# Kernel tuning notes

Measured on AMD Instinct MI355X. Metric: run time of the kernel, lower is better.

Reference implementation:

```python
import jax, jax.numpy as jnp
import numpy as np

N = 1024   # num nodes (assets)
F = 128    # node feature dim (node_dim)
M = 256    # memory_dim (scorer hidden)
E = 8      # edge_dim
BN_EPS = 1e-5


def setup_inputs() -> dict:
    key = jax.random.key(0)
    ks = jax.random.split(key, 6)
    x = jax.random.normal(ks[0], (N, F), dtype=jnp.float32)
    ctx = jax.random.uniform(ks[1], (4,), dtype=jnp.float32)  # [crisis_prob, ttc/30, urgency, confidence]
    W1 = jax.random.normal(ks[2], (M, 2 * F + 4), dtype=jnp.float32) * 0.05
    b1 = jnp.zeros((M,), jnp.float32)
    gamma = jnp.ones((M,), jnp.float32)
    beta = jnp.zeros((M,), jnp.float32)
    run_mean = jnp.zeros((M,), jnp.float32)
    run_var = jnp.ones((M,), jnp.float32)
    W2 = jax.random.normal(ks[3], (E, M), dtype=jnp.float32) * 0.05
    b2 = jnp.zeros((E,), jnp.float32)
    W3 = jax.random.normal(ks[4], (1, E), dtype=jnp.float32) * 0.05
    b3 = jnp.zeros((1,), jnp.float32)
    return {"x": x, "ctx": ctx, "W1": W1, "b1": b1, "gamma": gamma, "beta": beta,
            "run_mean": run_mean, "run_var": run_var, "W2": W2, "b2": b2, "W3": W3, "b3": b3}


def reference(x, ctx, W1, b1, gamma, beta, run_mean, run_var, W2, b2, W3, b3):
    # All unordered pairs i<j (static shapes); original loops over stressed pairs only,
    # we score all pairs and expose the stressed/threshold filter as a boolean mask.
    ii, jj = jnp.triu_indices(N, k=1)  # each [P], P = N*(N-1)/2

    # First linear decomposed: W1 @ [x_i; x_j; ctx] = A x_i + B x_j + (C ctx + b1)
    pa = x @ W1[:, :F].T          # [N, M]
    pb = x @ W1[:, F:2 * F].T     # [N, M]
    cterm = ctx @ W1[:, 2 * F:].T + b1  # [M]

    h = jax.nn.relu(pa[ii] + pb[jj] + cterm)                           # [P, M]
    h = gamma * (h - run_mean) * jax.lax.rsqrt(run_var + BN_EPS) + beta  # eval-mode BatchNorm1d
    h = jax.nn.relu(h @ W2.T + b2)                                     # [P, E]
    scores = jax.nn.sigmoid(h @ W3.T + b3)[:, 0]                       # [P]

    # Stressed-node selection: std over feature dim > mean std (torch unbiased std)
    stress = x.std(axis=1, ddof=1)
    stressed = stress > stress.mean()
    edge_mask = (scores > 0.5) & stressed[ii] & stressed[jj]           # [P] bool
    return scores, edge_mask
```

## Files before the change

kernel.cpp:

```cpp
#include <hip/hip_runtime.h>
#include <math.h>

#define N_NODES 1024
#define F_DIM   128
#define M_DIM   256
#define E_DIM   8
#define P_PAIRS 523776

__global__ __launch_bounds__(256) void kA(const float* __restrict__ x,
                                          const float* __restrict__ ctx,
                                          const float* __restrict__ W1,
                                          const float* __restrict__ b1,
                                          const float* __restrict__ gamma,
                                          const float* __restrict__ beta,
                                          const float* __restrict__ rmean,
                                          const float* __restrict__ rvar,
                                          const float* __restrict__ W2,
                                          const float* __restrict__ b2,
                                          float* __restrict__ pa,
                                          float* __restrict__ pb,
                                          float* __restrict__ stress,
                                          float* __restrict__ cterm,
                                          float* __restrict__ w2ft,
                                          float* __restrict__ b2f) {
  const int t = threadIdx.x;

  if (blockIdx.x == 256) {
    __shared__ float bnbs[256];
    const float c0 = ctx[0], c1 = ctx[1], c2 = ctx[2], c3 = ctx[3];
    const float* row = W1 + (size_t)t * 260 + 256;
    cterm[t] = b1[t] + c0 * row[0] + c1 * row[1] + c2 * row[2] + c3 * row[3];
    const float s   = gamma[t] / sqrtf(rvar[t] + 1e-5f);
    bnbs[t] = beta[t] - s * rmean[t];
    #pragma unroll
    for (int e = 0; e < 8; ++e) w2ft[t * 8 + e] = W2[e * 256 + t] * s;
    __syncthreads();
    const int wv = t >> 6, lane = t & 63;
    #pragma unroll
    for (int r = 0; r < 2; ++r) {
      const int e = wv * 2 + r;
      float acc = 0.f;
      #pragma unroll
      for (int k = 0; k < 4; ++k) acc += W2[e * 256 + lane + 64 * k] * bnbs[lane + 64 * k];
      #pragma unroll
      for (int m = 32; m > 0; m >>= 1) acc += __shfl_xor(acc, m, 64);
      if (lane == 0) b2f[e] = acc + b2[e];
    }
    return;
  }

  __shared__ float xv[4][128];
  const int n0 = blockIdx.x * 4;
  if (t < 128) {
    ((float4*)&xv[0][0])[t] = ((const float4*)(x + (size_t)n0 * F_DIM))[t];
  }
  __syncthreads();

  {
    const int wv = t >> 6, lane = t & 63;
    const float a = xv[wv][lane], b = xv[wv][lane + 64];
    float sum = a + b;
    #pragma unroll
    for (int m = 32; m > 0; m >>= 1) sum += __shfl_xor(sum, m, 64);
    const float mean = sum * (1.0f / 128.0f);
    const float d0 = a - mean, d1 = b - mean;
    float ss = d0 * d0 + d1 * d1;
    #pragma unroll
    for (int m = 32; m > 0; m >>= 1) ss += __shfl_xor(ss, m, 64);
    if (lane == 0) stress[n0 + wv] = sqrtf(ss * (1.0f / 127.0f));
  }

  const int m = t;
  const float4* wrow = (const float4*)(W1 + (size_t)m * 260);
  float accA[4] = {0.f, 0.f, 0.f, 0.f};
  float accB[4] = {0.f, 0.f, 0.f, 0.f};
  #pragma unroll 8
  for (int k4 = 0; k4 < 32; ++k4) {
    const float4 wa = wrow[k4];
    const float4 wb = wrow[32 + k4];
    #pragma unroll
    for (int nn = 0; nn < 4; ++nn) {
      const float4 xf = ((const float4*)&xv[nn][0])[k4];
      accA[nn] = fmaf(xf.w, wa.w, fmaf(xf.z, wa.z, fmaf(xf.y, wa.y, fmaf(xf.x, wa.x, accA[nn]))));
      accB[nn] = fmaf(xf.w, wb.w, fmaf(xf.z, wb.z, fmaf(xf.y, wb.y, fmaf(xf.x, wb.x, accB[nn]))));
    }
  }
  #pragma unroll
  for (int nn = 0; nn < 4; ++nn) {
    pa[(size_t)(n0 + nn) * M_DIM + m] = accA[nn];
    pb[(size_t)(n0 + nn) * M_DIM + m] = accB[nn];
  }
}

__global__ __launch_bounds__(256, 5) void kC(const float* __restrict__ pa,
                                             const float* __restrict__ pb,
                                             const float* __restrict__ cterm,
                                             const float* __restrict__ w2ft,
                                             const float* __restrict__ b2f,
                                             const float* __restrict__ W3,
                                             const float* __restrict__ b3,
                                             const float* __restrict__ stress,
                                             float* __restrict__ out) {
  const int ti = blockIdx.x, tj = blockIdx.y;
  if (tj < ti) return;
  __shared__ float4 a4[32 * 32];
  __shared__ float4 b4[32 * 32];
  const int t  = threadIdx.x;
  const int i0 = ti * 32, j0 = tj * 32;

  float ssum = 0.f;
  {
    const int lane = t & 63;
    #pragma unroll
    for (int k = 0; k < 16; ++k) ssum += stress[lane + 64 * k];
    #pragma unroll
    for (int m = 32; m > 0; m >>= 1) ssum += __shfl_xor(ssum, m, 64);
  }
  const float smean = ssum * (1.0f / 1024.0f);

  const int jx = t & 15;
  const int iy = t >> 4;
  float acc[4][8];
  #pragma unroll
  for (int p = 0; p < 4; ++p)
    #pragma unroll
    for (int e = 0; e < 8; ++e) acc[p][e] = 0.f;

  const float4* pa4 = (const float4*)pa;
  const float4* pb4 = (const float4*)pb;
  const float4* ct4 = (const float4*)cterm;
  const float4* w4g = (const float4*)w2ft;

  for (int cb = 0; cb < 2; ++cb) {
    if (cb) __syncthreads();
    #pragma unroll
    for (int p = 0; p < 4; ++p) {
      const int d  = p * 256 + t;
      const int r  = d >> 5;
      const int dc = d & 31;
      const int c  = (dc - r) & 31;
      const float4 cv = ct4[cb * 32 + c];
      float4 av = pa4[(size_t)(i0 + r) * 64 + cb * 32 + c];
      av.x += cv.x; av.y += cv.y; av.z += cv.z; av.w += cv.w;
      a4[d] = av;
      b4[d] = pb4[(size_t)(j0 + r) * 64 + cb * 32 + c];
    }
    __syncthreads();

    #pragma unroll 2
    for (int m4 = 0; m4 < 32; ++m4) {
      const float4 a0 = a4[iy * 32        + ((m4 + iy) & 31)];
      const float4 a1 = a4[(iy + 16) * 32 + ((m4 + iy + 16) & 31)];
      const float4 b0 = b4[jx * 32        + ((m4 + jx) & 31)];
      const float4 b1 = b4[(jx + 16) * 32 + ((m4 + jx + 16) & 31)];
      float4 w[8];
      #pragma unroll
      for (int q = 0; q < 8; ++q) w[q] = w4g[(cb * 32 + m4) * 8 + q];

      const float* a0f = (const float*)&a0;
      const float* a1f = (const float*)&a1;
      const float* b0f = (const float*)&b0;
      const float* b1f = (const float*)&b1;
      #pragma unroll
      for (int mm = 0; mm < 4; ++mm) {
        const float r00 = fmaxf(a0f[mm] + b0f[mm], 0.f);
        const float r01 = fmaxf(a0f[mm] + b1f[mm], 0.f);
        const float r10 = fmaxf(a1f[mm] + b0f[mm], 0.f);
        const float r11 = fmaxf(a1f[mm] + b1f[mm], 0.f);
        const float* wl = (const float*)&w[mm * 2];
        const float* wh = (const float*)&w[mm * 2 + 1];
        #pragma unroll
        for (int e = 0; e < 4; ++e) {
          acc[0][e]     = fmaf(wl[e], r00, acc[0][e]);
          acc[1][e]     = fmaf(wl[e], r01, acc[1][e]);
          acc[2][e]     = fmaf(wl[e], r10, acc[2][e]);
          acc[3][e]     = fmaf(wl[e], r11, acc[3][e]);
          acc[0][e + 4] = fmaf(wh[e], r00, acc[0][e + 4]);
          acc[1][e + 4] = fmaf(wh[e], r01, acc[1][e + 4]);
          acc[2][e + 4] = fmaf(wh[e], r10, acc[2][e + 4]);
          acc[3][e + 4] = fmaf(wh[e], r11, acc[3][e + 4]);
        }
      }
    }
  }

  float w3v[8], b2v[8];
  #pragma unroll
  for (int e = 0; e < 8; ++e) { w3v[e] = W3[e]; b2v[e] = b2f[e]; }
  const float b3v = b3[0];
  #pragma unroll
  for (int ia = 0; ia < 2; ++ia) {
    #pragma unroll
    for (int jb = 0; jb < 2; ++jb) {
      const int i = i0 + iy + ia * 16;
      const int j = j0 + jx + jb * 16;
      if (i < j) {
        const int p = ia * 2 + jb;
        float logit = b3v;
        #pragma unroll
        for (int e = 0; e < 8; ++e) {
          const float h2 = fmaxf(acc[p][e] + b2v[e], 0.f);
          logit = fmaf(w3v[e], h2, logit);
        }
        const float score = 1.0f / (1.0f + expf(-logit));
        const int idx = i * 1023 - (i * (i - 1)) / 2 + (j - i - 1);
        out[idx] = score;
        const bool mk = (score > 0.5f) && (stress[i] > smean) && (stress[j] > smean);
        out[P_PAIRS + idx] = mk ? 1.0f : 0.0f;
      }
    }
  }
}

extern "C" void kernel_launch(void* const* d_in, const int* in_sizes, int n_in,
                              void* d_out, int out_size, void* d_ws, size_t ws_size,
                              hipStream_t stream) {
  const float* x     = (const float*)d_in[0];
  const float* ctx   = (const float*)d_in[1];
  const float* W1    = (const float*)d_in[2];
  const float* b1    = (const float*)d_in[3];
  const float* gamma = (const float*)d_in[4];
  const float* beta  = (const float*)d_in[5];
  const float* rmean = (const float*)d_in[6];
  const float* rvar  = (const float*)d_in[7];
  const float* W2    = (const float*)d_in[8];
  const float* b2    = (const float*)d_in[9];
  const float* W3    = (const float*)d_in[10];
  const float* b3    = (const float*)d_in[11];
  float* out = (float*)d_out;

  float* ws     = (float*)d_ws;
  float* pa     = ws;
  float* pb     = pa + 262144;
  float* cterm  = pb + 262144;
  float* w2ft   = cterm + 256;
  float* b2f    = w2ft + 2048;
  float* stress = b2f + 8;

  hipLaunchKernelGGL(kA, dim3(257), dim3(256), 0, stream, x, ctx, W1, b1, gamma, beta,
                     rmean, rvar, W2, b2, pa, pb, stress, cterm, w2ft, b2f);
  hipLaunchKernelGGL(kC, dim3(32, 32), dim3(256), 0, stream, pa, pb, cterm, w2ft, b2f,
                     W3, b3, stress, out);
}
```

Baseline: 145.7 us.

## Compact triangular tile grid, fold ctx term into pa, prefetch second chunk

The pair kernel now launches only the 528 upper-triangular 32x32 tiles and recovers (ti,tj) from the linear block index with a sqrt. This replaces the 1024-block grid in which almost half the blocks exited immediately. The context/bias term is now added into pa inside the projection kernel, so the separate cterm buffer and its per-load adds are gone. The second feature chunk is loaded into registers while the first chunk computes, hiding global load latency. The occupancy hint drops from 5 to 4 blocks to make room for the extra prefetch registers, and the inner loop unroll rises to 4.

```diff
diff --git a/kernel.cpp b/kernel.cpp
--- a/kernel.cpp
+++ b/kernel.cpp
@@ -6,6 +6,7 @@
 #define M_DIM   256
 #define E_DIM   8
 #define P_PAIRS 523776
+#define NTILES  528
 
 __global__ __launch_bounds__(256) void kA(const float* __restrict__ x,
                                           const float* __restrict__ ctx,
@@ -20,16 +21,12 @@
                                           float* __restrict__ pa,
                                           float* __restrict__ pb,
                                           float* __restrict__ stress,
-                                          float* __restrict__ cterm,
                                           float* __restrict__ w2ft,
                                           float* __restrict__ b2f) {
   const int t = threadIdx.x;
 
   if (blockIdx.x == 256) {
     __shared__ float bnbs[256];
-    const float c0 = ctx[0], c1 = ctx[1], c2 = ctx[2], c3 = ctx[3];
-    const float* row = W1 + (size_t)t * 260 + 256;
-    cterm[t] = b1[t] + c0 * row[0] + c1 * row[1] + c2 * row[2] + c3 * row[3];
     const float s   = gamma[t] / sqrtf(rvar[t] + 1e-5f);
     bnbs[t] = beta[t] - s * rmean[t];
     #pragma unroll
@@ -85,27 +82,33 @@
       accB[nn] = fmaf(xf.w, wb.w, fmaf(xf.z, wb.z, fmaf(xf.y, wb.y, fmaf(xf.x, wb.x, accB[nn]))));
     }
   }
+  const float c0 = ctx[0], c1 = ctx[1], c2 = ctx[2], c3 = ctx[3];
+  const float* rowt = W1 + (size_t)m * 260 + 256;
+  const float ctv = b1[m] + c0 * rowt[0] + c1 * rowt[1] + c2 * rowt[2] + c3 * rowt[3];
   #pragma unroll
   for (int nn = 0; nn < 4; ++nn) {
-    pa[(size_t)(n0 + nn) * M_DIM + m] = accA[nn];
+    pa[(size_t)(n0 + nn) * M_DIM + m] = accA[nn] + ctv;
     pb[(size_t)(n0 + nn) * M_DIM + m] = accB[nn];
   }
 }
 
-__global__ __launch_bounds__(256, 5) void kC(const float* __restrict__ pa,
+__global__ __launch_bounds__(256, 4) void kC(const float* __restrict__ pa,
                                              const float* __restrict__ pb,
-                                             const float* __restrict__ cterm,
                                              const float* __restrict__ w2ft,
                                              const float* __restrict__ b2f,
                                              const float* __restrict__ W3,
                                              const float* __restrict__ b3,
                                              const float* __restrict__ stress,
                                              float* __restrict__ out) {
-  const int ti = blockIdx.x, tj = blockIdx.y;
-  if (tj < ti) return;
   __shared__ float4 a4[32 * 32];
   __shared__ float4 b4[32 * 32];
-  const int t  = threadIdx.x;
+  const int t = threadIdx.x;
+
+  const int p = blockIdx.x;
+  int tj = (int)((sqrtf(8.0f * (float)p + 1.0f) - 1.0f) * 0.5f);
+  while ((tj + 1) * (tj + 2) / 2 <= p) ++tj;
+  while (tj * (tj + 1) / 2 > p) --tj;
+  const int ti = p - tj * (tj + 1) / 2;
   const int i0 = ti * 32, j0 = tj * 32;
 
   float ssum = 0.f;
@@ -122,32 +125,39 @@
   const int iy = t >> 4;
   float acc[4][8];
   #pragma unroll
-  for (int p = 0; p < 4; ++p)
-    #pragma unroll
-    for (int e = 0; e < 8; ++e) acc[p][e] = 0.f;
+  for (int q = 0; q < 4; ++q)
+    #pragma unroll
+    for (int e = 0; e < 8; ++e) acc[q][e] = 0.f;
 
   const float4* pa4 = (const float4*)pa;
   const float4* pb4 = (const float4*)pb;
-  const float4* ct4 = (const float4*)cterm;
   const float4* w4g = (const float4*)w2ft;
 
-  for (int cb = 0; cb < 2; ++cb) {
-    if (cb) __syncthreads();
-    #pragma unroll
-    for (int p = 0; p < 4; ++p) {
-      const int d  = p * 256 + t;
-      const int r  = d >> 5;
-      const int dc = d & 31;
-      const int c  = (dc - r) & 31;
-      const float4 cv = ct4[cb * 32 + c];
-      float4 av = pa4[(size_t)(i0 + r) * 64 + cb * 32 + c];
-      av.x += cv.x; av.y += cv.y; av.z += cv.z; av.w += cv.w;
-      a4[d] = av;
-      b4[d] = pb4[(size_t)(j0 + r) * 64 + cb * 32 + c];
-    }
-    __syncthreads();
-
-    #pragma unroll 2
+  float4 ra[4], rb[4];
+
+  #pragma unroll
+  for (int q = 0; q < 4; ++q) {
+    const int d = q * 256 + t, r = d >> 5, dc = d & 31, c = (dc - r) & 31;
+    ra[q] = pa4[(size_t)(i0 + r) * 64 + c];
+    rb[q] = pb4[(size_t)(j0 + r) * 64 + c];
+  }
+  #pragma unroll
+  for (int q = 0; q < 4; ++q) {
+    const int d = q * 256 + t;
+    a4[d] = ra[q];
+    b4[d] = rb[q];
+  }
+  __syncthreads();
+
+  #pragma unroll
+  for (int q = 0; q < 4; ++q) {
+    const int d = q * 256 + t, r = d >> 5, dc = d & 31, c = (dc - r) & 31;
+    ra[q] = pa4[(size_t)(i0 + r) * 64 + 32 + c];
+    rb[q] = pb4[(size_t)(j0 + r) * 64 + 32 + c];
+  }
+
+  auto computeChunk = [&](int cw) {
+    #pragma unroll 4
     for (int m4 = 0; m4 < 32; ++m4) {
       const float4 a0 = a4[iy * 32        + ((m4 + iy) & 31)];
       const float4 a1 = a4[(iy + 16) * 32 + ((m4 + iy + 16) & 31)];
@@ -155,7 +165,7 @@
       const float4 b1 = b4[(jx + 16) * 32 + ((m4 + jx + 16) & 31)];
       float4 w[8];
       #pragma unroll
-      for (int q = 0; q < 8; ++q) w[q] = w4g[(cb * 32 + m4) * 8 + q];
+      for (int q = 0; q < 8; ++q) w[q] = w4g[(cw + m4) * 8 + q];
 
       const float* a0f = (const float*)&a0;
       const float* a1f = (const float*)&a1;
@@ -182,7 +192,18 @@
         }
       }
     }
-  }
+  };
+
+  computeChunk(0);
+  __syncthreads();
+  #pragma unroll
+  for (int q = 0; q < 4; ++q) {
+    const int d = q * 256 + t;
+    a4[d] = ra[q];
+    b4[d] = rb[q];
+  }
+  __syncthreads();
+  computeChunk(32);
 
   float w3v[8], b2v[8];
   #pragma unroll
@@ -195,11 +216,11 @@
       const int i = i0 + iy + ia * 16;
       const int j = j0 + jx + jb * 16;
       if (i < j) {
-        const int p = ia * 2 + jb;
+        const int q = ia * 2 + jb;
         float logit = b3v;
         #pragma unroll
         for (int e = 0; e < 8; ++e) {
-          const float h2 = fmaxf(acc[p][e] + b2v[e], 0.f);
+          const float h2 = fmaxf(acc[q][e] + b2v[e], 0.f);
           logit = fmaf(w3v[e], h2, logit);
         }
         const float score = 1.0f / (1.0f + expf(-logit));
@@ -232,13 +253,12 @@
   float* ws     = (float*)d_ws;
   float* pa     = ws;
   float* pb     = pa + 262144;
-  float* cterm  = pb + 262144;
-  float* w2ft   = cterm + 256;
+  float* w2ft   = pb + 262144;
   float* b2f    = w2ft + 2048;
   float* stress = b2f + 8;
 
   hipLaunchKernelGGL(kA, dim3(257), dim3(256), 0, stream, x, ctx, W1, b1, gamma, beta,
-                     rmean, rvar, W2, b2, pa, pb, stress, cterm, w2ft, b2f);
-  hipLaunchKernelGGL(kC, dim3(32, 32), dim3(256), 0, stream, pa, pb, cterm, w2ft, b2f,
+                     rmean, rvar, W2, b2, pa, pb, stress, w2ft, b2f);
+  hipLaunchKernelGGL(kC, dim3(NTILES), dim3(256), 0, stream, pa, pb, w2ft, b2f,
                      W3, b3, stress, out);
 }
```

New measurement: 135.9 us. -6.7%, faster.
